# Kernel tuning notes

Measured on AMD Instinct MI355X. Metric: run time of the kernel, lower is better.

The kernel has to match this reference:

```python
import jax, jax.numpy as jnp
import numpy as np

H = 2048
V = 32000
B = 4            # 2 chosen + 2 rejected sequences
T = 1024
BETA = 0.1
IGNORE_INDEX = -100


def setup_inputs() -> dict:
    key = jax.random.key(0)
    k1, k2, k3, k4, k5 = jax.random.split(key, 5)
    x = jax.random.normal(k1, (B, T, H), dtype=jnp.float32)
    ref_x = jax.random.normal(k2, (B, T, H), dtype=jnp.float32)
    y = jax.random.randint(k3, (B, T), 0, V, dtype=jnp.int64)
    # Linear weights scaled ~1/sqrt(H) so logits are well-conditioned
    W = jax.random.normal(k4, (V, H), dtype=jnp.float32) * (1.0 / np.sqrt(H))
    W_ref = jax.random.normal(k5, (V, H), dtype=jnp.float32) * (1.0 / np.sqrt(H))
    return {"x": x, "ref_x": ref_x, "y": y, "W": W, "W_ref": W_ref}


def _avg_seq_logps(h, W, y, mask):
    # h: [B,T,H], W: [V,H] -> average per-sequence log-prob of the target tokens
    logits = jnp.einsum("bth,vh->btv", h, W)                 # [B,T,V]
    logps = jax.nn.log_softmax(logits, axis=-1)
    y_safe = jnp.where(mask, y, 0)
    per_tok = jnp.take_along_axis(logps, y_safe[..., None], axis=-1)[..., 0]  # [B,T]
    m = mask.astype(logps.dtype)
    return (per_tok * m).sum(-1) / m.sum(-1)                  # [B]


def reference(x, ref_x, y, W, W_ref):
    mask = y != IGNORE_INDEX
    logps = _avg_seq_logps(x, W, y, mask)
    # reference model path is computed without gradients (torch.no_grad in Liger)
    ref_logps = jax.lax.stop_gradient(_avg_seq_logps(ref_x, W_ref, y, mask))
    half = B // 2
    chosen, rejected = logps[:half], logps[half:]
    ref_chosen, ref_rejected = ref_logps[:half], ref_logps[half:]
    logits_diff = BETA * ((chosen - ref_chosen) - (rejected - ref_rejected))
    loss = -jax.nn.log_sigmoid(logits_diff).sum() / half
    return loss
```

## Files before the change

kernel.cpp:

```cpp
#include <hip/hip_runtime.h>
#include <cstdint>
#include <cstddef>

#define HDIM 2048
#define VOCAB 32000
#define BT 4096
#define NVB 125
#define BETA_F 0.1f
#define SCALE_X 16.0f
#define SCALE_W 64.0f
#define INV_SC (1.0f / (SCALE_X * SCALE_W))

typedef float f32x4 __attribute__((ext_vector_type(4)));
typedef long lx2 __attribute__((ext_vector_type(2)));

__device__ __forceinline__ void async_lds16(const void* g, void* l) {
  __builtin_amdgcn_global_load_lds(
      (__attribute__((address_space(1))) void*)g,
      (__attribute__((address_space(3))) void*)l,
      16, 0, 0);
}

#define BAR() __builtin_amdgcn_s_barrier()
#define SCHED0() __builtin_amdgcn_sched_barrier(0)
#define VMCNT(n) do { asm volatile("s_waitcnt vmcnt(" #n ")" ::: "memory"); \
                      __builtin_amdgcn_sched_barrier(0); } while (0)

__global__ void cast_fp8_kernel(const float* __restrict__ src,
                                uint4* __restrict__ dst, int n16, float scale) {
  int i = blockIdx.x * blockDim.x + threadIdx.x;
  int stride = gridDim.x * blockDim.x;
  for (; i < n16; i += stride) {
    const float4* s = (const float4*)src + (size_t)i * 4;
    uint4 o;
    {
      float4 a = s[0];
      int r = __builtin_amdgcn_cvt_pk_fp8_f32(a.x * scale, a.y * scale, 0, false);
      o.x = __builtin_amdgcn_cvt_pk_fp8_f32(a.z * scale, a.w * scale, r, true);
    }
    {
      float4 a = s[1];
      int r = __builtin_amdgcn_cvt_pk_fp8_f32(a.x * scale, a.y * scale, 0, false);
      o.y = __builtin_amdgcn_cvt_pk_fp8_f32(a.z * scale, a.w * scale, r, true);
    }
    {
      float4 a = s[2];
      int r = __builtin_amdgcn_cvt_pk_fp8_f32(a.x * scale, a.y * scale, 0, false);
      o.z = __builtin_amdgcn_cvt_pk_fp8_f32(a.z * scale, a.w * scale, r, true);
    }
    {
      float4 a = s[3];
      int r = __builtin_amdgcn_cvt_pk_fp8_f32(a.x * scale, a.y * scale, 0, false);
      o.w = __builtin_amdgcn_cvt_pk_fp8_f32(a.z * scale, a.w * scale, r, true);
    }
    dst[i] = o;
  }
}

__global__ __launch_bounds__(1024) void gemm_lse256(
    const unsigned char* __restrict__ Xq,
    const unsigned char* __restrict__ Xrq,
    const unsigned char* __restrict__ Wq,
    const unsigned char* __restrict__ Wrq,
    float2* __restrict__ part) {
  __shared__ __align__(16) char lds[2][2][2][8192];

  const int tid = threadIdx.x;
  const int lane = tid & 63;
  const int w = tid >> 6;
  const int wm = w >> 2;
  const int wn = w & 3;
  const int which = blockIdx.y;

  const int lin = blockIdx.x;
  const int nl = (lin & 7) * 250 + (lin >> 3);
  const int mb = nl & 15;
  const int nb = nl >> 4;

  const unsigned char* A = which ? Xrq : Xq;
  const unsigned char* B = which ? Wrq : Wq;
  float2* pp = part + (size_t)which * BT * NVB;

  const int lanep = lane ^ ((lane & 32) >> 4);
  const int srow = (w >> 3) * 128 + (w & 7) * 16 + (lanep >> 2);
  const int scol = (lanep & 3) * 16;
  const unsigned char* Ag = A + (size_t)(mb * 256 + srow) * HDIM + scol;
  const unsigned char* Bg = B + (size_t)(nb * 256 + srow) * HDIM + scol;

#define STAGE_AB(buf, T) do {                                                 \
    async_lds16(Ag + (size_t)(T) * 64, &lds[buf][0][0][0] + w * 1024);        \
    async_lds16(Bg + (size_t)(T) * 64, &lds[buf][1][0][0] + w * 1024);        \
  } while (0)

  const int l15 = lane & 15;
  const int kbyte = (lane >> 4) * 16;
#define FRAGP(d0, d1, halfptr, row) do {                                      \
    int _r = (row);                                                           \
    int _L = _r * 64 + kbyte;                                                 \
    lx2 _v = *(const lx2*)((halfptr) + (_L ^ (((_r >> 3) & 1) << 5)));        \
    d0 = _v.x; d1 = _v.y;                                                     \
  } while (0)

  const char* Ah[2] = { &lds[0][0][wm >> 1][0], &lds[1][0][wm >> 1][0] };
  const char* Bh[2] = { &lds[0][1][wn >> 1][0], &lds[1][1][wn >> 1][0] };
  const int arow = (wm & 1) * 64 + l15;
  const int brow = (wn & 1) * 64 + l15;

  f32x4 acc[4][4] = {};
  long aLo[2][2], aHi[2][2], bLo[2][2], bHi[2][2];

#define RD_ALO(buf) do {                                                      \
    _Pragma("unroll") for (int mi = 0; mi < 2; ++mi)                          \
      FRAGP(aLo[mi][0], aLo[mi][1], Ah[buf], arow + mi * 16);                 \
  } while (0)
#define RD_AHI(buf) do {                                                      \
    _Pragma("unroll") for (int mi = 0; mi < 2; ++mi)                          \
      FRAGP(aHi[mi][0], aHi[mi][1], Ah[buf], arow + (2 + mi) * 16);           \
  } while (0)
#define RD_B01(buf) do {                                                      \
    _Pragma("unroll") for (int ni = 0; ni < 2; ++ni)                          \
      FRAGP(bLo[ni][0], bLo[ni][1], Bh[buf], brow + ni * 16);                 \
  } while (0)
#define RD_B23(buf) do {                                                      \
    _Pragma("unroll") for (int ni = 0; ni < 2; ++ni)                          \
      FRAGP(bHi[ni][0], bHi[ni][1], Bh[buf], brow + (2 + ni) * 16);           \
  } while (0)
#define MFMA_Q(AG, BG, MI0, NI0) do {                                         \
    __builtin_amdgcn_s_setprio(1);                                            \
    _Pragma("unroll") for (int kk = 0; kk < 2; ++kk)                          \
    _Pragma("unroll") for (int mi = 0; mi < 2; ++mi)                          \
    _Pragma("unroll") for (int ni = 0; ni < 2; ++ni)                          \
      acc[(MI0) + mi][(NI0) + ni] = __builtin_amdgcn_mfma_f32_16x16x32_fp8_fp8( \
          AG[mi][kk], BG[ni][kk], acc[(MI0) + mi][(NI0) + ni], 0, 0, 0);      \
    __builtin_amdgcn_s_setprio(0);                                            \
  } while (0)

  STAGE_AB(0, 0);
  STAGE_AB(1, 1);
  VMCNT(2);
  BAR(); SCHED0();
  RD_ALO(0); RD_B01(0);
  SCHED0();

  for (int i = 0; i < 16; ++i) {
    const int se = (2 * i + 2 > 30) ? 30 : 2 * i + 2;
    const int so = (2 * i + 3 > 31) ? 31 : 2 * i + 3;

    RD_B23(0); SCHED0();
    MFMA_Q(aLo, bLo, 0, 0); SCHED0();
    RD_AHI(0); SCHED0();
    MFMA_Q(aLo, bHi, 0, 2); SCHED0();
    MFMA_Q(aHi, bLo, 2, 0); SCHED0();
    VMCNT(0);
    BAR(); SCHED0();
    STAGE_AB(0, se);
    RD_ALO(1); RD_B01(1); SCHED0();
    MFMA_Q(aHi, bHi, 2, 2); SCHED0();

    RD_B23(1); SCHED0();
    MFMA_Q(aLo, bLo, 0, 0); SCHED0();
    RD_AHI(1); SCHED0();
    MFMA_Q(aLo, bHi, 0, 2); SCHED0();
    MFMA_Q(aHi, bLo, 2, 0); SCHED0();
    VMCNT(0);
    BAR(); SCHED0();
    STAGE_AB(1, so);
    RD_ALO(0); RD_B01(0); SCHED0();
    MFMA_Q(aHi, bHi, 2, 2); SCHED0();
  }
  VMCNT(0);
  BAR(); SCHED0();

  float* red = (float*)&lds[0][0][0][0];
#pragma unroll
  for (int mi = 0; mi < 4; ++mi) {
#pragma unroll
    for (int r = 0; r < 4; ++r) {
      float v0 = acc[mi][0][r] * INV_SC;
      float v1 = acc[mi][1][r] * INV_SC;
      float v2 = acc[mi][2][r] * INV_SC;
      float v3 = acc[mi][3][r] * INV_SC;
      float m = fmaxf(fmaxf(v0, v1), fmaxf(v2, v3));
#pragma unroll
      for (int o = 1; o < 16; o <<= 1) m = fmaxf(m, __shfl_xor(m, o, 64));
      float s = __expf(v0 - m) + __expf(v1 - m) + __expf(v2 - m) + __expf(v3 - m);
#pragma unroll
      for (int o = 1; o < 16; o <<= 1) s += __shfl_xor(s, o, 64);
      if (l15 == 0) {
        int row = wm * 64 + mi * 16 + (lane >> 4) * 4 + r;
        red[wn * 256 + row] = m;
        red[1024 + wn * 256 + row] = s;
      }
    }
  }
  __syncthreads();
  if (tid < 256) {
    float m0 = red[tid], m1 = red[256 + tid], m2 = red[512 + tid], m3 = red[768 + tid];
    float M = fmaxf(fmaxf(m0, m1), fmaxf(m2, m3));
    float S = red[1024 + tid] * __expf(m0 - M) + red[1280 + tid] * __expf(m1 - M) +
              red[1536 + tid] * __expf(m2 - M) + red[1792 + tid] * __expf(m3 - M);
    pp[(size_t)(mb * 256 + tid) * NVB + nb] = make_float2(M, S);
  }
#undef STAGE_AB
#undef FRAGP
#undef RD_ALO
#undef RD_AHI
#undef RD_B01
#undef RD_B23
#undef MFMA_Q
}

__global__ void target_logit(const float* __restrict__ x, const float* __restrict__ xr,
                             const float* __restrict__ W, const float* __restrict__ Wr,
                             const int* __restrict__ y, float* __restrict__ tlog) {
  int wid = (blockIdx.x * blockDim.x + threadIdx.x) >> 6;
  int lane = threadIdx.x & 63;
  int which = wid >> 12;
  int tok = wid & 4095;
  int yy = y[tok];
  int ys = (yy == -100) ? 0 : yy;
  const float* xv = (which ? xr : x) + (size_t)tok * HDIM;
  const float* wv = (which ? Wr : W) + (size_t)ys * HDIM;
  const float4* x4 = (const float4*)xv;
  const float4* w4 = (const float4*)wv;
  float sum = 0.f;
  for (int i = lane; i < HDIM / 4; i += 64) {
    float4 a = x4[i], b = w4[i];
    sum += a.x * b.x + a.y * b.y + a.z * b.z + a.w * b.w;
  }
#pragma unroll
  for (int o = 1; o < 64; o <<= 1) sum += __shfl_xor(sum, o, 64);
  if (lane == 0) tlog[wid] = sum;
}

__global__ void lse_combine(const float2* __restrict__ part,
                            const float* __restrict__ tlog,
                            float* __restrict__ ptok) {
  int wid = (blockIdx.x * blockDim.x + threadIdx.x) >> 6;
  int lane = threadIdx.x & 63;
  const float2* p = part + (size_t)wid * NVB;
  float m = -INFINITY, s = 0.f;
  for (int i = lane; i < NVB; i += 64) {
    float2 v = p[i];
    float M = fmaxf(m, v.x);
    s = s * __expf(m - M) + v.y * __expf(v.x - M);
    m = M;
  }
#pragma unroll
  for (int o = 1; o < 64; o <<= 1) {
    float mo = __shfl_xor(m, o, 64);
    float so = __shfl_xor(s, o, 64);
    float M = fmaxf(m, mo);
    s = s * __expf(m - M) + so * __expf(mo - M);
    m = M;
  }
  if (lane == 0) ptok[wid] = tlog[wid] - (m + logf(s));
}

__global__ void final_loss(const float* __restrict__ ptok,
                           const int* __restrict__ y, float* __restrict__ out) {
  __shared__ float rs[256];
  __shared__ float rc[256];
  __shared__ float seq[8];
  int tid = threadIdx.x;
  for (int s = 0; s < 8; ++s) {
    int which = s >> 2, b = s & 3;
    float lsum = 0.f, lcnt = 0.f;
    for (int t = tid; t < 1024; t += 256) {
      int yy = y[b * 1024 + t];
      if (yy != -100) {
        lsum += ptok[which * 4096 + b * 1024 + t];
        lcnt += 1.f;
      }
    }
    rs[tid] = lsum; rc[tid] = lcnt;
    __syncthreads();
    for (int o = 128; o > 0; o >>= 1) {
      if (tid < o) { rs[tid] += rs[tid + o]; rc[tid] += rc[tid + o]; }
      __syncthreads();
    }
    if (tid == 0) seq[s] = rs[0] / rc[0];
    __syncthreads();
  }
  if (tid == 0) {
    float d0 = BETA_F * ((seq[0] - seq[4]) - (seq[2] - seq[6]));
    float d1 = BETA_F * ((seq[1] - seq[5]) - (seq[3] - seq[7]));
    auto sp = [](float a) { return fmaxf(a, 0.f) + log1pf(expf(-fabsf(a))); };
    out[0] = (sp(-d0) + sp(-d1)) * 0.5f;
  }
}

extern "C" void kernel_launch(void* const* d_in, const int* in_sizes, int n_in,
                              void* d_out, int out_size, void* d_ws, size_t ws_size,
                              hipStream_t stream) {
  const float* x   = (const float*)d_in[0];
  const float* xr  = (const float*)d_in[1];
  const int*   y   = (const int*)d_in[2];
  const float* Wf  = (const float*)d_in[3];
  const float* Wrf = (const float*)d_in[4];
  float* out = (float*)d_out;

  char* ws = (char*)d_ws;
  size_t off = 0;
  auto alloc = [&](size_t bytes) -> void* {
    void* p = ws + off;
    off = (off + bytes + 255) & ~(size_t)255;
    return p;
  };
  unsigned char* Xq  = (unsigned char*)alloc((size_t)BT * HDIM);
  unsigned char* Xrq = (unsigned char*)alloc((size_t)BT * HDIM);
  unsigned char* Wq  = (unsigned char*)alloc((size_t)VOCAB * HDIM);
  unsigned char* Wrq = (unsigned char*)alloc((size_t)VOCAB * HDIM);
  float2* part = (float2*)alloc((size_t)2 * BT * NVB * sizeof(float2));
  float*  tlog = (float*)alloc((size_t)2 * BT * sizeof(float));
  float*  ptok = (float*)alloc((size_t)2 * BT * sizeof(float));

  cast_fp8_kernel<<<2048, 256, 0, stream>>>(x,  (uint4*)Xq,  BT * HDIM / 16, SCALE_X);
  cast_fp8_kernel<<<2048, 256, 0, stream>>>(xr, (uint4*)Xrq, BT * HDIM / 16, SCALE_X);
  cast_fp8_kernel<<<2048, 256, 0, stream>>>(Wf,  (uint4*)Wq,  VOCAB * HDIM / 16, SCALE_W);
  cast_fp8_kernel<<<2048, 256, 0, stream>>>(Wrf, (uint4*)Wrq, VOCAB * HDIM / 16, SCALE_W);

  dim3 gg(2000, 2);
  gemm_lse256<<<gg, 1024, 0, stream>>>(Xq, Xrq, Wq, Wrq, part);

  target_logit<<<2048, 256, 0, stream>>>(x, xr, Wf, Wrf, y, tlog);
  lse_combine<<<2048, 256, 0, stream>>>(part, tlog, ptok);
  final_loss<<<1, 256, 0, stream>>>(ptok, y, out);
}
```

Baseline: 934.5 us.

## Deepen LDS pipeline to four stages with prefetch distance three

Raises the shared-memory ring for the FP8 GEMM from two to four buffers and issues async global-to-LDS loads three tiles ahead, placing the next load early in each tile and waiting with vmcnt(4) instead of draining to zero. This aims to hide global load latency behind more MFMA work and stop each iteration from stalling on the tile just requested. It doubles LDS usage to 128 KB per block and issues redundant clamped loads at the end of the loop.

```diff
diff --git a/kernel.cpp b/kernel.cpp
--- a/kernel.cpp
+++ b/kernel.cpp
@@ -63,7 +63,7 @@
     const unsigned char* __restrict__ Wq,
     const unsigned char* __restrict__ Wrq,
     float2* __restrict__ part) {
-  __shared__ __align__(16) char lds[2][2][2][8192];
+  __shared__ __align__(16) char lds[4][2][2][8192];
 
   const int tid = threadIdx.x;
   const int lane = tid & 63;
@@ -88,8 +88,9 @@
   const unsigned char* Bg = B + (size_t)(nb * 256 + srow) * HDIM + scol;
 
 #define STAGE_AB(buf, T) do {                                                 \
-    async_lds16(Ag + (size_t)(T) * 64, &lds[buf][0][0][0] + w * 1024);        \
-    async_lds16(Bg + (size_t)(T) * 64, &lds[buf][1][0][0] + w * 1024);        \
+    int _t = (T) > 31 ? 31 : (T);                                             \
+    async_lds16(Ag + (size_t)_t * 64, &lds[buf][0][0][0] + w * 1024);         \
+    async_lds16(Bg + (size_t)_t * 64, &lds[buf][1][0][0] + w * 1024);         \
   } while (0)
 
   const int l15 = lane & 15;
@@ -101,8 +102,10 @@
     d0 = _v.x; d1 = _v.y;                                                     \
   } while (0)
 
-  const char* Ah[2] = { &lds[0][0][wm >> 1][0], &lds[1][0][wm >> 1][0] };
-  const char* Bh[2] = { &lds[0][1][wn >> 1][0], &lds[1][1][wn >> 1][0] };
+  const char* Ah[4] = { &lds[0][0][wm >> 1][0], &lds[1][0][wm >> 1][0],
+                        &lds[2][0][wm >> 1][0], &lds[3][0][wm >> 1][0] };
+  const char* Bh[4] = { &lds[0][1][wn >> 1][0], &lds[1][1][wn >> 1][0],
+                        &lds[2][1][wn >> 1][0], &lds[3][1][wn >> 1][0] };
   const int arow = (wm & 1) * 64 + l15;
   const int brow = (wn & 1) * 64 + l15;
 
@@ -135,38 +138,33 @@
     __builtin_amdgcn_s_setprio(0);                                            \
   } while (0)
 
+#define TILE(C, CN, ST) do {                                                  \
+    RD_B23(C); SCHED0();                                                      \
+    MFMA_Q(aLo, bLo, 0, 0); SCHED0();                                         \
+    STAGE_AB((C + 3) & 3, ST);                                                \
+    RD_AHI(C); SCHED0();                                                      \
+    MFMA_Q(aLo, bHi, 0, 2); SCHED0();                                         \
+    MFMA_Q(aHi, bLo, 2, 0); SCHED0();                                         \
+    VMCNT(4);                     \
+    BAR(); SCHED0();                                                          \
+    RD_ALO(CN); RD_B01(CN); SCHED0();                                         \
+    MFMA_Q(aHi, bHi, 2, 2); SCHED0();                                         \
+  } while (0)
+
   STAGE_AB(0, 0);
   STAGE_AB(1, 1);
-  VMCNT(2);
+  STAGE_AB(2, 2);
+  VMCNT(4);
   BAR(); SCHED0();
   RD_ALO(0); RD_B01(0);
   SCHED0();
 
-  for (int i = 0; i < 16; ++i) {
-    const int se = (2 * i + 2 > 30) ? 30 : 2 * i + 2;
-    const int so = (2 * i + 3 > 31) ? 31 : 2 * i + 3;
-
-    RD_B23(0); SCHED0();
-    MFMA_Q(aLo, bLo, 0, 0); SCHED0();
-    RD_AHI(0); SCHED0();
-    MFMA_Q(aLo, bHi, 0, 2); SCHED0();
-    MFMA_Q(aHi, bLo, 2, 0); SCHED0();
-    VMCNT(0);
-    BAR(); SCHED0();
-    STAGE_AB(0, se);
-    RD_ALO(1); RD_B01(1); SCHED0();
-    MFMA_Q(aHi, bHi, 2, 2); SCHED0();
-
-    RD_B23(1); SCHED0();
-    MFMA_Q(aLo, bLo, 0, 0); SCHED0();
-    RD_AHI(1); SCHED0();
-    MFMA_Q(aLo, bHi, 0, 2); SCHED0();
-    MFMA_Q(aHi, bLo, 2, 0); SCHED0();
-    VMCNT(0);
-    BAR(); SCHED0();
-    STAGE_AB(1, so);
-    RD_ALO(0); RD_B01(0); SCHED0();
-    MFMA_Q(aHi, bHi, 2, 2); SCHED0();
+  for (int i = 0; i < 8; ++i) {
+    const int base = 4 * i;
+    TILE(0, 1, base + 3);
+    TILE(1, 2, base + 4);
+    TILE(2, 3, base + 5);
+    TILE(3, 0, base + 6);
   }
   VMCNT(0);
   BAR(); SCHED0();
@@ -208,6 +206,7 @@
 #undef RD_B01
 #undef RD_B23
 #undef MFMA_Q
+#undef TILE
 }
 
 __global__ void target_logit(const float* __restrict__ x, const float* __restrict__ xr,
```

Measured after the change: 1.111 ms. 1.19x slower.
